# Kernel tuning notes

Hardware: AMD Instinct MI355X
Metric: run time of the kernel (lower is better)

Reference implementation:

```python
import jax, jax.numpy as jnp
import numpy as np

B, S, E, H = 2, 2048, 1024, 16
D = E // H  # head_dim = 64
FE = 4      # forward_expansion
EPS = 1e-5


def layernorm(x, g, b):
    mu = jnp.mean(x, axis=-1, keepdims=True)
    var = jnp.var(x, axis=-1, keepdims=True)
    return (x - mu) * jax.lax.rsqrt(var + EPS) * g + b


def setup_inputs() -> dict:
    key = jax.random.key(0)
    ks = jax.random.split(key, 16)
    s = lambda d: 1.0 / np.sqrt(d)
    return {
        "queries": jax.random.normal(ks[0], (B, S, E), jnp.float32),
        "keys": jax.random.normal(ks[1], (B, S, E), jnp.float32),
        "values": jax.random.normal(ks[2], (B, S, E), jnp.float32),
        "mask": jnp.ones((B, 1, S, S), jnp.int32),  # ignored (faithful to source bug)
        "Wq": jax.random.normal(ks[3], (D, D), jnp.float32) * s(D),
        "Wk": jax.random.normal(ks[4], (D, D), jnp.float32) * s(D),
        "Wv": jax.random.normal(ks[5], (D, D), jnp.float32) * s(D),
        "Wfc": jax.random.normal(ks[6], (E, E), jnp.float32) * s(E),
        "bfc": jnp.zeros((E,), jnp.float32),
        "W1": jax.random.normal(ks[7], (FE * E, E), jnp.float32) * s(E),
        "b1": jnp.zeros((FE * E,), jnp.float32),
        "W2": jax.random.normal(ks[8], (E, FE * E), jnp.float32) * s(FE * E),
        "b2": jnp.zeros((E,), jnp.float32),
        "ln1_g": jnp.ones((E,), jnp.float32),
        "ln1_b": jnp.zeros((E,), jnp.float32),
        "ln2_g": jnp.ones((E,), jnp.float32),
        "ln2_b": jnp.zeros((E,), jnp.float32),
    }


def reference(queries, keys, values, mask, Wq, Wk, Wv, Wfc, bfc, W1, b1, W2, b2,
              ln1_g, ln1_b, ln2_g, ln2_b):
    # --- MHA ---
    q = queries.reshape(B, S, H, D) @ Wq.T  # [B,S,H,D]
    k = keys.reshape(B, S, H, D) @ Wk.T
    v = values.reshape(B, S, H, D) @ Wv.T
    scores = jnp.einsum('bqhd,bkhd->bhqk', q, k)
    # source: softmax(scores / S**(-1/2)) == scores * sqrt(S)  (faithful quirk)
    # mask is ignored: source masked_fill is non-inplace and discarded
    attn = jax.nn.softmax(scores * jnp.sqrt(jnp.float32(S)), axis=-1)
    out = jnp.einsum('bhqk,bkhd->bqhd', attn, v).reshape(B, S, E)
    att = out @ Wfc.T + bfc
    # --- residual + LN + FFN + LN (dropout p=0 -> identity) ---
    h = layernorm(att + queries, ln1_g, ln1_b)
    x = jax.nn.relu(h @ W1.T + b1) @ W2.T + b2
    return layernorm(x + h, ln2_g, ln2_b)
```

## Files before the change

### kernel.cpp

```cpp
#include <hip/hip_runtime.h>
#include <hip/hip_bf16.h>
#include <math.h>

#define B_ 2
#define S_ 2048
#define E_ 1024
#define H_ 16
#define D_ 64
#define TOK (B_*S_)
#define SCALE2 (45.254833995939045f * 1.44269504088896340f)

typedef __bf16 bf16x8 __attribute__((ext_vector_type(8)));
typedef float floatx4 __attribute__((ext_vector_type(4)));
struct b4s { __hip_bfloat16 x, y, z, w; };

typedef const __attribute__((address_space(1))) char ga_char;
typedef __attribute__((address_space(3))) char ls_char;

__device__ __forceinline__ void gload_lds16(const void* g, ls_char* l) {
  __builtin_amdgcn_global_load_lds((ga_char*)g, l, 16, 0, 0);
}

#if __has_builtin(__builtin_amdgcn_exp2f)
#define EXP2(x) __builtin_amdgcn_exp2f(x)
#else
#define EXP2(x) exp2f(x)
#endif

#define SWZ(arr, half, row, qpos) \
  (*(bf16x8*)&arr[half][row][(((qpos) ^ ((row) & 3)) * 8)])

__device__ __forceinline__ void sbar() {
  asm volatile("" ::: "memory");
  __builtin_amdgcn_s_barrier();
  asm volatile("" ::: "memory");
}
#define VMW(n) asm volatile("s_waitcnt vmcnt(" #n ")" ::: "memory")

__global__ __launch_bounds__(256) void cast_all(
    const float* __restrict__ Wfc, const float* __restrict__ W1,
    const float* __restrict__ W2, __hip_bfloat16* __restrict__ Wfcb,
    __hip_bfloat16* __restrict__ W1b, __hip_bfloat16* __restrict__ W2b,
    const float* __restrict__ Wq, const float* __restrict__ Wk,
    const float* __restrict__ Wv, __hip_bfloat16* __restrict__ Whl) {
  const int i = blockIdx.x * 256 + threadIdx.x;
  if (i < 2359296) {
    const float* src; __hip_bfloat16* dst; int j;
    if (i < 262144)       { src = Wfc; dst = Wfcb; j = i; }
    else if (i < 1310720) { src = W1;  dst = W1b;  j = i - 262144; }
    else                  { src = W2;  dst = W2b;  j = i - 1310720; }
    float4 v = ((const float4*)src)[j];
    b4s o;
    o.x = __float2bfloat16(v.x); o.y = __float2bfloat16(v.y);
    o.z = __float2bfloat16(v.z); o.w = __float2bfloat16(v.w);
    *(b4s*)(dst + (size_t)j * 4) = o;
  } else if (i < 2362368) {
    const int idx = i - 2359296;
    const int m = idx >> 10;
    const int off = (idx & 1023) * 4;
    const float* W = (m == 0) ? Wq : (m == 1) ? Wk : Wv;
    float4 v = *(const float4*)(W + off);
    b4s hi, lo;
    hi.x = __float2bfloat16(v.x); lo.x = __float2bfloat16(v.x - __bfloat162float(hi.x));
    hi.y = __float2bfloat16(v.y); lo.y = __float2bfloat16(v.y - __bfloat162float(hi.y));
    hi.z = __float2bfloat16(v.z); lo.z = __float2bfloat16(v.z - __bfloat162float(hi.z));
    hi.w = __float2bfloat16(v.w); lo.w = __float2bfloat16(v.w - __bfloat162float(hi.w));
    *(b4s*)(Whl + (size_t)m * 8192 + off) = hi;
    *(b4s*)(Whl + (size_t)m * 8192 + 4096 + off) = lo;
  }
}

__global__ __launch_bounds__(256) void qkv_fused(
    const float* __restrict__ xq, const float* __restrict__ xk,
    const float* __restrict__ xv, const __hip_bfloat16* __restrict__ Whl,
    __hip_bfloat16* __restrict__ qhi, __hip_bfloat16* __restrict__ qlo,
    __hip_bfloat16* __restrict__ khi, __hip_bfloat16* __restrict__ klo,
    __hip_bfloat16* __restrict__ vt) {
  __shared__ __bf16 Xh[2][64][32], Xl[2][64][32];
  __shared__ __bf16 Vt[64][72];
  const int t = threadIdx.x, lane = t & 63, w = t >> 6;
  const int quad = lane >> 4, low = lane & 15;
  const int bh = blockIdx.y;
  const int b = bh >> 4, h = bh & 15;
  const int s0 = blockIdx.x * 64;
  const int sr = t >> 2;
  const int sc = (t & 3) * 16;
  const int scc = sc >> 5;
  const int p0 = (sc & 31) >> 3;

  for (int m = 0; m < 3; m++) {
    const float* xin = (m == 0) ? xq : (m == 1) ? xk : xv;
    const __hip_bfloat16* Wh = Whl + (size_t)m * 8192;
    const float sc_m = (m == 0) ? SCALE2 : 1.0f;

    __syncthreads();
    {
      const float* src = xin + ((size_t)(b * S_ + s0 + sr)) * E_ + h * 64 + sc;
      float4 f0 = *(const float4*)(src);
      float4 f1 = *(const float4*)(src + 4);
      float4 f2 = *(const float4*)(src + 8);
      float4 f3 = *(const float4*)(src + 12);
      float fv[16] = {f0.x, f0.y, f0.z, f0.w, f1.x, f1.y, f1.z, f1.w,
                      f2.x, f2.y, f2.z, f2.w, f3.x, f3.y, f3.z, f3.w};
      bf16x8 hi0, hi1, lo0, lo1;
      #pragma unroll
      for (int j = 0; j < 8; j++) {
        hi0[j] = (__bf16)fv[j];
        lo0[j] = (__bf16)(fv[j] - (float)hi0[j]);
        hi1[j] = (__bf16)fv[8 + j];
        lo1[j] = (__bf16)(fv[8 + j] - (float)hi1[j]);
      }
      SWZ(Xh, scc, sr, p0) = hi0;
      SWZ(Xh, scc, sr, p0 + 1) = hi1;
      SWZ(Xl, scc, sr, p0) = lo0;
      SWZ(Xl, scc, sr, p0 + 1) = lo1;
    }
    __syncthreads();

    bf16x8 ah[2], al[2];
    #pragma unroll
    for (int c = 0; c < 2; c++) {
      ah[c] = SWZ(Xh, c, w * 16 + low, quad);
      al[c] = SWZ(Xl, c, w * 16 + low, quad);
    }

    floatx4 acc[4];
    #pragma unroll
    for (int nn = 0; nn < 4; nn++) {
      floatx4 a = {};
      #pragma unroll
      for (int c = 0; c < 2; c++) {
        const __hip_bfloat16* wp = Wh + (nn * 16 + low) * 64 + c * 32 + quad * 8;
        bf16x8 wh_ = *(const bf16x8*)wp;
        bf16x8 wl_ = *(const bf16x8*)(wp + 4096);
        a = __builtin_amdgcn_mfma_f32_16x16x32_bf16(ah[c], wh_, a, 0, 0, 0);
        a = __builtin_amdgcn_mfma_f32_16x16x32_bf16(al[c], wh_, a, 0, 0, 0);
        a = __builtin_amdgcn_mfma_f32_16x16x32_bf16(ah[c], wl_, a, 0, 0, 0);
      }
      acc[nn] = a;
    }

    if (m < 2) {
      __hip_bfloat16* dh = (m == 0) ? qhi : khi;
      __hip_bfloat16* dl = (m == 0) ? qlo : klo;
      #pragma unroll
      for (int nn = 0; nn < 4; nn++) {
        #pragma unroll
        for (int i = 0; i < 4; i++) {
          const int s = s0 + w * 16 + quad * 4 + i;
          const int d = nn * 16 + low;
          const size_t adr = ((size_t)bh * S_ + s) * 64 + d;
          const float f = acc[nn][i] * sc_m;
          const __hip_bfloat16 hb = __float2bfloat16(f);
          dh[adr] = hb;
          dl[adr] = __float2bfloat16(f - __bfloat162float(hb));
        }
      }
    } else {
      #pragma unroll
      for (int nn = 0; nn < 4; nn++)
        #pragma unroll
        for (int i = 0; i < 4; i++)
          Vt[nn * 16 + low][w * 16 + quad * 4 + i] = (__bf16)acc[nn][i];
      __syncthreads();
      const int dr = t >> 2;
      const int scl = (t & 3) * 16;
      __hip_bfloat16* dst = vt + ((size_t)bh * 64 + dr) * S_ + s0 + scl;
      bf16x8 o0 = *(const bf16x8*)&Vt[dr][scl];
      bf16x8 o1 = *(const bf16x8*)&Vt[dr][scl + 8];
      *(bf16x8*)dst = o0;
      *(bf16x8*)(dst + 8) = o1;
    }
  }
}

__device__ __forceinline__ void softmax_update(
    const floatx4* sa, floatx4* oacc, float& mrow, float& lrow, bf16x8* pb) {
  float rmax;
  {
    float m0 = fmaxf(fmaxf(sa[0][0], sa[0][1]), fmaxf(sa[0][2], sa[0][3]));
    float m1 = fmaxf(fmaxf(sa[1][0], sa[1][1]), fmaxf(sa[1][2], sa[1][3]));
    float m2 = fmaxf(fmaxf(sa[2][0], sa[2][1]), fmaxf(sa[2][2], sa[2][3]));
    float m3 = fmaxf(fmaxf(sa[3][0], sa[3][1]), fmaxf(sa[3][2], sa[3][3]));
    rmax = fmaxf(fmaxf(m0, m1), fmaxf(m2, m3));
    rmax = fmaxf(rmax, __shfl_xor(rmax, 16, 64));
    rmax = fmaxf(rmax, __shfl_xor(rmax, 32, 64));
  }
  if (__any(rmax > mrow)) {
    const float nm = fmaxf(mrow, rmax);
    const float al = EXP2(mrow - nm);
    mrow = nm;
    lrow *= al;
    #pragma unroll
    for (int dt = 0; dt < 4; dt++) {
      oacc[dt][0] *= al; oacc[dt][1] *= al;
      oacc[dt][2] *= al; oacc[dt][3] *= al;
    }
  }
  float p[4][4];
  float rs;
  {
    float r0_ = 0.f, r1_ = 0.f, r2_ = 0.f, r3_ = 0.f;
    #pragma unroll
    for (int i = 0; i < 4; i++) {
      p[0][i] = EXP2(sa[0][i] - mrow); r0_ += p[0][i];
      p[1][i] = EXP2(sa[1][i] - mrow); r1_ += p[1][i];
      p[2][i] = EXP2(sa[2][i] - mrow); r2_ += p[2][i];
      p[3][i] = EXP2(sa[3][i] - mrow); r3_ += p[3][i];
    }
    rs = (r0_ + r1_) + (r2_ + r3_);
    rs += __shfl_xor(rs, 16, 64);
    rs += __shfl_xor(rs, 32, 64);
  }
  lrow += rs;
  #pragma unroll
  for (int kh2 = 0; kh2 < 2; kh2++) {
    bf16x8 v;
    v[0] = (__bf16)p[kh2][0]; v[1] = (__bf16)p[kh2][1];
    v[2] = (__bf16)p[kh2][2]; v[3] = (__bf16)p[kh2][3];
    v[4] = (__bf16)p[kh2 + 2][0]; v[5] = (__bf16)p[kh2 + 2][1];
    v[6] = (__bf16)p[kh2 + 2][2]; v[7] = (__bf16)p[kh2 + 2][3];
    pb[kh2] = v;
  }
}

__global__ __launch_bounds__(512, 4) void attn_mfma(
    const __hip_bfloat16* __restrict__ Qhi, const __hip_bfloat16* __restrict__ Qlo,
    const __hip_bfloat16* __restrict__ Khi, const __hip_bfloat16* __restrict__ Klo,
    const __hip_bfloat16* __restrict__ Vtg, __hip_bfloat16* __restrict__ ctx) {
  __shared__ __bf16 Kh[2][2][64][32], Kl[2][2][64][32], Vs[2][2][64][32];
  const int t = threadIdx.x, lane = t & 63, w = t >> 6;
  const int quad = lane >> 4, low = lane & 15;
  const int bh = blockIdx.x;
  const int qw = blockIdx.y * 128 + w * 16;

  const int sh = w >> 2;
  const int r0 = (w & 3) * 16;
  const int srow = r0 + (lane >> 2);
  const int sq = (lane & 3) ^ (srow & 3);
  const __hip_bfloat16* gK = Khi + ((size_t)bh * S_ + srow) * 64 + sh * 32 + sq * 8;
  const __hip_bfloat16* gL = Klo + ((size_t)bh * S_ + srow) * 64 + sh * 32 + sq * 8;
  const __hip_bfloat16* gV = Vtg + ((size_t)bh * 64 + srow) * S_ + sh * 32 + sq * 8;

  bf16x8 qh[2], ql[2];
  {
    const size_t qbase = ((size_t)bh * S_ + qw + low) * 64 + quad * 8;
    qh[0] = *(const bf16x8*)(Qhi + qbase);
    qh[1] = *(const bf16x8*)(Qhi + qbase + 32);
    ql[0] = *(const bf16x8*)(Qlo + qbase);
    ql[1] = *(const bf16x8*)(Qlo + qbase + 32);
  }

  floatx4 oacc[4] = {};
  float mrow = -3e38f, lrow = 0.f;

  gload_lds16(gK, (ls_char*)&Kh[0][sh][r0][0]);
  gload_lds16(gL, (ls_char*)&Kl[0][sh][r0][0]);
  gload_lds16(gV, (ls_char*)&Vs[0][sh][r0][0]);

  for (int kt = 0; kt < S_ / 64; kt++) {
    const int cur = kt & 1;
    __syncthreads();
    if (kt + 1 < S_ / 64) {
      gload_lds16(gK + (size_t)(kt + 1) * 4096, (ls_char*)&Kh[cur ^ 1][sh][r0][0]);
      gload_lds16(gL + (size_t)(kt + 1) * 4096, (ls_char*)&Kl[cur ^ 1][sh][r0][0]);
      gload_lds16(gV + (size_t)(kt + 1) * 64,   (ls_char*)&Vs[cur ^ 1][sh][r0][0]);
    }

    floatx4 sa[4];
    __builtin_amdgcn_s_setprio(1);
    #pragma unroll
    for (int nn = 0; nn < 4; nn++) {
      const int prow = (nn & 1) * 32 + (nn >> 1) * 4 + (low >> 2) * 8 + (low & 3);
      bf16x8 kh0 = SWZ(Kh[cur], 0, prow, quad);
      bf16x8 kh1 = SWZ(Kh[cur], 1, prow, quad);
      bf16x8 kl0 = SWZ(Kl[cur], 0, prow, quad);
      bf16x8 kl1 = SWZ(Kl[cur], 1, prow, quad);
      floatx4 s = {};
      s = __builtin_amdgcn_mfma_f32_16x16x32_bf16(kh0, qh[0], s, 0, 0, 0);
      s = __builtin_amdgcn_mfma_f32_16x16x32_bf16(kh1, qh[1], s, 0, 0, 0);
      s = __builtin_amdgcn_mfma_f32_16x16x32_bf16(kl0, qh[0], s, 0, 0, 0);
      s = __builtin_amdgcn_mfma_f32_16x16x32_bf16(kl1, qh[1], s, 0, 0, 0);
      s = __builtin_amdgcn_mfma_f32_16x16x32_bf16(kh0, ql[0], s, 0, 0, 0);
      s = __builtin_amdgcn_mfma_f32_16x16x32_bf16(kh1, ql[1], s, 0, 0, 0);
      sa[nn] = s;
    }
    __builtin_amdgcn_s_setprio(0);

    bf16x8 pb[2];
    softmax_update(sa, oacc, mrow, lrow, pb);

    __builtin_amdgcn_s_setprio(1);
    #pragma unroll
    for (int dt = 0; dt < 4; dt++) {
      bf16x8 vb0 = SWZ(Vs[cur], 0, dt * 16 + low, quad);
      bf16x8 vb1 = SWZ(Vs[cur], 1, dt * 16 + low, quad);
      oacc[dt] = __builtin_amdgcn_mfma_f32_16x16x32_bf16(vb0, pb[0], oacc[dt], 0, 0, 0);
      oacc[dt] = __builtin_amdgcn_mfma_f32_16x16x32_bf16(vb1, pb[1], oacc[dt], 0, 0, 0);
    }
    __builtin_amdgcn_s_setprio(0);
  }

  const float inv = 1.0f / lrow;
  const int b = bh >> 4, h = bh & 15;
  const size_t base = ((size_t)(b * S_ + qw + low)) * E_ + h * 64 + quad * 4;
  #pragma unroll
  for (int dt = 0; dt < 4; dt++) {
    b4s o;
    o.x = __float2bfloat16(oacc[dt][0] * inv);
    o.y = __float2bfloat16(oacc[dt][1] * inv);
    o.z = __float2bfloat16(oacc[dt][2] * inv);
    o.w = __float2bfloat16(oacc[dt][3] * inv);
    *(b4s*)(ctx + base + dt * 16) = o;
  }
}

template <int RELU, int OUT_BF16, int PARTIAL>
__global__ __launch_bounds__(256) void gemm_mfma(
    const __hip_bfloat16* __restrict__ A, const __hip_bfloat16* __restrict__ Wt,
    const float* __restrict__ bias, void* __restrict__ C0, void* __restrict__ C1,
    int M, int N, int Kblk, int lda) {
  __shared__ __bf16 As[2][128][64];
  __shared__ __bf16 Bs[2][128][64];
  const int t = threadIdx.x;
  const int lane = t & 63;
  const int w = t >> 6;
  const int wr = w >> 1, wc = w & 1;
  const int m0 = blockIdx.y * 128, n0 = blockIdx.x * 128;
  void* Cout = (blockIdx.z == 0) ? C0 : C1;

  A += (size_t)blockIdx.z * Kblk;
  Wt += (size_t)blockIdx.z * Kblk;

  floatx4 acc[4][4] = {};
  const int srow = t >> 3;
  const int ssc = ((t & 7) ^ (srow & 7)) * 8;

  const __hip_bfloat16* gA = A + (size_t)(m0 + srow) * lda + ssc;
  const __hip_bfloat16* gB = Wt + (size_t)(n0 + srow) * lda + ssc;
  const size_t rstep = (size_t)32 * lda;

#define GSTAGE(buf, k0) do {                                      \
    ls_char* lA = (ls_char*)&As[buf][0][0] + w * 1024;            \
    ls_char* lB = (ls_char*)&Bs[buf][0][0] + w * 1024;            \
    gload_lds16(gA + (k0),             lA);                       \
    gload_lds16(gA + (k0) + rstep,     lA + 4096);                \
    gload_lds16(gA + (k0) + 2 * rstep, lA + 8192);                \
    gload_lds16(gA + (k0) + 3 * rstep, lA + 12288);               \
    gload_lds16(gB + (k0),             lB);                       \
    gload_lds16(gB + (k0) + rstep,     lB + 4096);                \
    gload_lds16(gB + (k0) + 2 * rstep, lB + 8192);                \
    gload_lds16(gB + (k0) + 3 * rstep, lB + 12288);               \
  } while (0)

  GSTAGE(0, 0);
  const int nsteps = Kblk >> 6;
  for (int st = 0; st < nsteps; st++) {
    const int cur = st & 1;
    __syncthreads();
    if (st + 1 < nsteps) GSTAGE(cur ^ 1, (st + 1) * 64);

    #pragma unroll
    for (int ks = 0; ks < 2; ks++) {
      bf16x8 af[4], bfr[4];
      #pragma unroll
      for (int i = 0; i < 4; i++) {
        const int ra = wr * 64 + i * 16 + (lane & 15);
        const int ca = (((lane >> 4) + ks * 4) ^ (ra & 7)) * 8;
        af[i] = *(const bf16x8*)&As[cur][ra][ca];
        const int rb = wc * 64 + i * 16 + (lane & 15);
        const int cb = (((lane >> 4) + ks * 4) ^ (rb & 7)) * 8;
        bfr[i] = *(const bf16x8*)&Bs[cur][rb][cb];
      }
      #pragma unroll
      for (int mi = 0; mi < 4; mi++)
        #pragma unroll
        for (int ni = 0; ni < 4; ni++)
          acc[mi][ni] = __builtin_amdgcn_mfma_f32_16x16x32_bf16(
              af[mi], bfr[ni], acc[mi][ni], 0, 0, 0);
    }
  }
#undef GSTAGE

  const int cil = lane & 15;
  const int quad = lane >> 4;
  #pragma unroll
  for (int ni = 0; ni < 4; ni++) {
    const int col = n0 + wc * 64 + ni * 16 + cil;
    const float bb = PARTIAL ? 0.f : bias[col];
    #pragma unroll
    for (int mi = 0; mi < 4; mi++) {
      const int row = m0 + wr * 64 + mi * 16 + quad * 4;
      #pragma unroll
      for (int i = 0; i < 4; i++) {
        if (PARTIAL) {
          ((float*)Cout)[(size_t)(row + i) * N + col] = acc[mi][ni][i];
        } else {
          float vv = acc[mi][ni][i] + bb;
          if (RELU) vv = fmaxf(vv, 0.f);
          if (OUT_BF16)
            ((__hip_bfloat16*)Cout)[(size_t)(row + i) * N + col] = __float2bfloat16(vv);
          else
            ((float*)Cout)[(size_t)(row + i) * N + col] = vv;
        }
      }
    }
  }
}

__global__ __launch_bounds__(512, 2) void gemm_ff1(
    const __hip_bfloat16* __restrict__ A, const __hip_bfloat16* __restrict__ Wt,
    const float* __restrict__ bias, __hip_bfloat16* __restrict__ C) {
  __shared__ __bf16 As[2][256][64];
  __shared__ __bf16 Bs[2][256][64];
  const int t = threadIdx.x, lane = t & 63, w = t >> 6;
  const int quad = lane >> 4, low = lane & 15;
  const int wm = w >> 2, wn = w & 3;
  const int m0 = blockIdx.y * 256, n0 = blockIdx.x * 256;

  floatx4 acc[8][4] = {};

  const int srow = t >> 3;
  const int ssc = ((t & 7) ^ (srow & 7)) * 8;
  const __hip_bfloat16* gA = A + (size_t)(m0 + srow) * 1024 + ssc;
  const __hip_bfloat16* gB = Wt + (size_t)(n0 + srow) * 1024 + ssc;

#define LA(buf) ((ls_char*)&As[buf][0][0] + w * 1024)
#define LB(buf) ((ls_char*)&Bs[buf][0][0] + w * 1024)
#define ST_A0(buf, k0) do {                                   \
    gload_lds16(gA + (k0),          LA(buf));                 \
    gload_lds16(gA + (k0) + 131072, LA(buf) + 16384);         \
  } while (0)
#define ST_A1(buf, k0) do {                                   \
    gload_lds16(gA + (k0) + 65536,  LA(buf) + 8192);          \
    gload_lds16(gA + (k0) + 196608, LA(buf) + 24576);         \
  } while (0)
#define ST_B0(buf, k0) do {                                   \
    gload_lds16(gB + (k0),          LB(buf));                 \
    gload_lds16(gB + (k0) + 65536,  LB(buf) + 8192);          \
  } while (0)
#define ST_B1(buf, k0) do {                                   \
    gload_lds16(gB + (k0) + 131072, LB(buf) + 16384);         \
    gload_lds16(gB + (k0) + 196608, LB(buf) + 24576);         \
  } while (0)

#define LDA_HALF(mh) do {                                                     \
    _Pragma("unroll")                                                         \
    for (int mi = 0; mi < 4; mi++) {                                          \
      const int ra = wm * 128 + (mh) * 64 + mi * 16 + low;                    \
      af[mi][0] = *(const bf16x8*)&As[cur][ra][((quad) ^ (ra & 7)) * 8];      \
      af[mi][1] = *(const bf16x8*)&As[cur][ra][((4 + quad) ^ (ra & 7)) * 8];  \
    }                                                                         \
  } while (0)

#define LDB_HALF(dst, nh) do {                                                \
    _Pragma("unroll")                                                         \
    for (int ni = 0; ni < 2; ni++) {                                          \
      const int rb = (nh) * 128 + wn * 32 + ni * 16 + low;                    \
      dst[ni][0] = *(const bf16x8*)&Bs[cur][rb][((quad) ^ (rb & 7)) * 8];     \
      dst[ni][1] = *(const bf16x8*)&Bs[cur][rb][((4 + quad) ^ (rb & 7)) * 8]; \
    }                                                                         \
  } while (0)

#define MFMA_Q(bfr, mh, nh) do {                                              \
    __builtin_amdgcn_s_setprio(1);                                            \
    _Pragma("unroll")                                                         \
    for (int mi = 0; mi < 4; mi++)                                            \
      _Pragma("unroll")                                                       \
      for (int ni = 0; ni < 2; ni++) {                                        \
        acc[(mh)*4+mi][(nh)*2+ni] = __builtin_amdgcn_mfma_f32_16x16x32_bf16(  \
            af[mi][0], bfr[ni][0], acc[(mh)*4+mi][(nh)*2+ni], 0, 0, 0);       \
        acc[(mh)*4+mi][(nh)*2+ni] = __builtin_amdgcn_mfma_f32_16x16x32_bf16(  \
            af[mi][1], bfr[ni][1], acc[(mh)*4+mi][(nh)*2+ni], 0, 0, 0);       \
      }                                                                       \
    __builtin_amdgcn_s_setprio(0);                                            \
  } while (0)

  ST_A0(0, 0); ST_B0(0, 0); ST_B1(0, 0); ST_A1(0, 0);

  bf16x8 af[4][2], bA[2][2], bB[2][2];

  for (int kt = 0; kt < 16; kt++) {
    const int cur = kt & 1, nxt = cur ^ 1;
    const int kn = (kt + 1) * 64;
    const bool more = (kt + 1 < 16);

    VMW(4);
    sbar();
    LDA_HALF(0);
    LDB_HALF(bA, 0);
    if (more) ST_A0(nxt, kn);
    MFMA_Q(bA, 0, 0);

    if (kt < 15) { VMW(4); } else { VMW(2); }
    sbar();
    LDB_HALF(bB, 1);
    if (more) ST_B0(nxt, kn);
    MFMA_Q(bB, 0, 1);

    if (kt < 15) { VMW(4); } else { VMW(0); }
    sbar();
    LDA_HALF(1);
    if (more) ST_B1(nxt, kn);
    MFMA_Q(bB, 1, 1);

    sbar();
    if (more) ST_A1(nxt, kn);
    MFMA_Q(bA, 1, 0);
  }
#undef ST_A0
#undef ST_A1
#undef ST_B0
#undef ST_B1
#undef LA
#undef LB
#undef LDA_HALF
#undef LDB_HALF
#undef MFMA_Q

  #pragma unroll
  for (int n4 = 0; n4 < 4; n4++) {
    const int nh = n4 >> 1, ni = n4 & 1;
    const int col = n0 + nh * 128 + wn * 32 + ni * 16 + low;
    const float bb = bias[col];
    #pragma unroll
    for (int mi = 0; mi < 8; mi++) {
      const int row = m0 + wm * 128 + mi * 16 + quad * 4;
      #pragma unroll
      for (int i = 0; i < 4; i++) {
        float vv = fmaxf(acc[mi][n4][i] + bb, 0.f);
        C[(size_t)(row + i) * 4096 + col] = __float2bfloat16(vv);
      }
    }
  }
}

template <int EMIT_BF16, int HAS_A1, int HAS_BIAS>
__global__ __launch_bounds__(256) void add_ln(
    const float* __restrict__ a0, const float* __restrict__ a1,
    const float* __restrict__ r, const float* __restrict__ bias,
    const float* __restrict__ g, const float* __restrict__ bt,
    float* __restrict__ out, __hip_bfloat16* __restrict__ outb) {
  __shared__ float red[16];
  const int tok = blockIdx.x, t = threadIdx.x;
  float4 av = ((const float4*)(a0 + (size_t)tok * E_))[t];
  float4 rv = ((const float4*)(r + (size_t)tok * E_))[t];
  float4 x;
  x.x = av.x + rv.x; x.y = av.y + rv.y; x.z = av.z + rv.z; x.w = av.w + rv.w;
  if (HAS_A1) {
    float4 a2 = ((const float4*)(a1 + (size_t)tok * E_))[t];
    x.x += a2.x; x.y += a2.y; x.z += a2.z; x.w += a2.w;
  }
  if (HAS_BIAS) {
    float4 cv = ((const float4*)bias)[t];
    x.x += cv.x; x.y += cv.y; x.z += cv.z; x.w += cv.w;
  }
  float sum = x.x + x.y + x.z + x.w;
  float ssq = x.x * x.x + x.y * x.y + x.z * x.z + x.w * x.w;
  #pragma unroll
  for (int off = 32; off >= 1; off >>= 1) {
    sum += __shfl_down(sum, off, 64);
    ssq += __shfl_down(ssq, off, 64);
  }
  const int wave = t >> 6;
  if ((t & 63) == 0) { red[wave] = sum; red[4 + wave] = ssq; }
  __syncthreads();
  if (t == 0) {
    float s = red[0] + red[1] + red[2] + red[3];
    float qq = red[4] + red[5] + red[6] + red[7];
    float mu = s * (1.0f / E_);
    red[8] = mu;
    red[9] = qq * (1.0f / E_) - mu * mu;
  }
  __syncthreads();
  const float mu = red[8];
  const float inv = rsqrtf(red[9] + 1e-5f);
  float4 gv = ((const float4*)g)[t];
  float4 bv = ((const float4*)bt)[t];
  float4 o;
  o.x = (x.x - mu) * inv * gv.x + bv.x;
  o.y = (x.y - mu) * inv * gv.y + bv.y;
  o.z = (x.z - mu) * inv * gv.z + bv.z;
  o.w = (x.w - mu) * inv * gv.w + bv.w;
  ((float4*)(out + (size_t)tok * E_))[t] = o;
  if (EMIT_BF16) {
    b4s ob;
    ob.x = __float2bfloat16(o.x); ob.y = __float2bfloat16(o.y);
    ob.z = __float2bfloat16(o.z); ob.w = __float2bfloat16(o.w);
    *(b4s*)(outb + (size_t)tok * E_ + t * 4) = ob;
  }
}

extern "C" void kernel_launch(void* const* d_in, const int* in_sizes, int n_in,
                              void* d_out, int out_size, void* d_ws, size_t ws_size,
                              hipStream_t stream) {
  const float* queries = (const float*)d_in[0];
  const float* keys    = (const float*)d_in[1];
  const float* values  = (const float*)d_in[2];
  const float* Wq  = (const float*)d_in[4];
  const float* Wk  = (const float*)d_in[5];
  const float* Wv  = (const float*)d_in[6];
  const float* Wfc = (const float*)d_in[7];
  const float* bfc = (const float*)d_in[8];
  const float* W1  = (const float*)d_in[9];
  const float* b1  = (const float*)d_in[10];
  const float* W2  = (const float*)d_in[11];
  const float* b2  = (const float*)d_in[12];
  const float* ln1_g = (const float*)d_in[13];
  const float* ln1_b = (const float*)d_in[14];
  const float* ln2_g = (const float*)d_in[15];
  const float* ln2_b = (const float*)d_in[16];

  const size_t M1 = 1048576;
  float* ws = (float*)d_ws;
  float* P0  = ws;
  float* P1  = ws + 4 * M1;
  float* Hf  = ws + 8 * M1;
  __hip_bfloat16* bb = (__hip_bfloat16*)(ws + 12 * M1);
  __hip_bfloat16* CTXb = bb;
  __hip_bfloat16* Hb   = bb + 4 * M1;
  __hip_bfloat16* Wfcb = bb + 8 * M1;
  __hip_bfloat16* W1b  = bb + 9 * M1;
  __hip_bfloat16* W2b  = bb + 13 * M1;
  __hip_bfloat16* Qhi  = bb + 17 * M1;
  __hip_bfloat16* Qlo  = bb + 21 * M1;
  __hip_bfloat16* Khi  = bb + 25 * M1;
  __hip_bfloat16* Klo  = bb + 29 * M1;
  __hip_bfloat16* Vtb  = bb + 33 * M1;
  __hip_bfloat16* FF1b = bb + 17 * M1;
  __hip_bfloat16* Whlb = bb + 37 * M1;
  float* out = (float*)d_out;

  cast_all<<<9228, 256, 0, stream>>>(Wfc, W1, W2, Wfcb, W1b, W2b,
                                     Wq, Wk, Wv, Whlb);

  qkv_fused<<<dim3(S_ / 64, B_ * H_), 256, 0, stream>>>(
      queries, keys, values, Whlb, Qhi, Qlo, Khi, Klo, Vtb);
  attn_mfma<<<dim3(B_ * H_, S_ / 128), 512, 0, stream>>>(
      Qhi, Qlo, Khi, Klo, Vtb, CTXb);
  gemm_mfma<0, 0, 1><<<dim3(E_ / 128, TOK / 128, 2), 256, 0, stream>>>(
      CTXb, Wfcb, nullptr, P0, P1, TOK, E_, 512, E_);
  add_ln<1, 1, 1><<<TOK, 256, 0, stream>>>(
      P0, P1, queries, bfc, ln1_g, ln1_b, Hf, Hb);
  gemm_ff1<<<dim3(4 * E_ / 256, TOK / 256), 512, 0, stream>>>(
      Hb, W1b, b1, FF1b);
  gemm_mfma<0, 0, 1><<<dim3(E_ / 128, TOK / 128, 2), 256, 0, stream>>>(
      FF1b, W2b, nullptr, P0, P1, TOK, E_, 2048, 4 * E_);
  add_ln<0, 1, 1><<<TOK, 256, 0, stream>>>(
      P0, P1, Hf, b2, ln2_g, ln2_b, out, nullptr);
}
```

Before: 377.2 us.

## Split GEMM K-tile into half-stages with finer-grained async LDS pipelining

Restructures the GEMM main loop so each 64-wide K tile is split into two 32-wide halves stored in separate LDS sub-buffers. Each half waits only on its own global-to-LDS loads via a partial vmcnt wait, issues the next tile's matching half-load, and then runs its MFMAs under raised wave priority. The aim is to overlap global loads with MFMA work more tightly and shorten load-to-use stalls. In exchange there are twice as many barriers per K step and a different swizzle layout, which could add synchronization overhead.

```diff
diff --git a/kernel.cpp b/kernel.cpp
--- a/kernel.cpp
+++ b/kernel.cpp
@@ -320,11 +320,12 @@
     const __hip_bfloat16* __restrict__ A, const __hip_bfloat16* __restrict__ Wt,
     const float* __restrict__ bias, void* __restrict__ C0, void* __restrict__ C1,
     int M, int N, int Kblk, int lda) {
-  __shared__ __bf16 As[2][128][64];
-  __shared__ __bf16 Bs[2][128][64];
+  __shared__ __bf16 As[2][2][128][32];
+  __shared__ __bf16 Bs[2][2][128][32];
   const int t = threadIdx.x;
   const int lane = t & 63;
   const int w = t >> 6;
+  const int quad = lane >> 4, low = lane & 15;
   const int wr = w >> 1, wc = w & 1;
   const int m0 = blockIdx.y * 128, n0 = blockIdx.x * 128;
   void* Cout = (blockIdx.z == 0) ? C0 : C1;
@@ -333,57 +334,75 @@
   Wt += (size_t)blockIdx.z * Kblk;
 
   floatx4 acc[4][4] = {};
-  const int srow = t >> 3;
-  const int ssc = ((t & 7) ^ (srow & 7)) * 8;
+  const int srow = t >> 2;
+  const int ssc = ((t & 3) ^ (srow & 3)) * 8;
 
   const __hip_bfloat16* gA = A + (size_t)(m0 + srow) * lda + ssc;
   const __hip_bfloat16* gB = Wt + (size_t)(n0 + srow) * lda + ssc;
-  const size_t rstep = (size_t)32 * lda;
-
-#define GSTAGE(buf, k0) do {                                      \
-    ls_char* lA = (ls_char*)&As[buf][0][0] + w * 1024;            \
-    ls_char* lB = (ls_char*)&Bs[buf][0][0] + w * 1024;            \
-    gload_lds16(gA + (k0),             lA);                       \
-    gload_lds16(gA + (k0) + rstep,     lA + 4096);                \
-    gload_lds16(gA + (k0) + 2 * rstep, lA + 8192);                \
-    gload_lds16(gA + (k0) + 3 * rstep, lA + 12288);               \
-    gload_lds16(gB + (k0),             lB);                       \
-    gload_lds16(gB + (k0) + rstep,     lB + 4096);                \
-    gload_lds16(gB + (k0) + 2 * rstep, lB + 8192);                \
-    gload_lds16(gB + (k0) + 3 * rstep, lB + 12288);               \
-  } while (0)
-
-  GSTAGE(0, 0);
+  const size_t rstep = (size_t)64 * lda;
+
+#define STA(buf, kh, k0) do {                                     \
+    ls_char* l = (ls_char*)&As[buf][kh][0][0] + w * 1024;         \
+    gload_lds16(gA + (k0),         l);                            \
+    gload_lds16(gA + (k0) + rstep, l + 4096);                     \
+  } while (0)
+#define STB(buf, kh, k0) do {                                     \
+    ls_char* l = (ls_char*)&Bs[buf][kh][0][0] + w * 1024;         \
+    gload_lds16(gB + (k0),         l);                            \
+    gload_lds16(gB + (k0) + rstep, l + 4096);                     \
+  } while (0)
+
+  STA(0, 0, 0); STB(0, 0, 0); STA(0, 1, 32); STB(0, 1, 32);
+
   const int nsteps = Kblk >> 6;
   for (int st = 0; st < nsteps; st++) {
-    const int cur = st & 1;
-    __syncthreads();
-    if (st + 1 < nsteps) GSTAGE(cur ^ 1, (st + 1) * 64);
-
-    #pragma unroll
-    for (int ks = 0; ks < 2; ks++) {
-      bf16x8 af[4], bfr[4];
-      #pragma unroll
-      for (int i = 0; i < 4; i++) {
-        const int ra = wr * 64 + i * 16 + (lane & 15);
-        const int ca = (((lane >> 4) + ks * 4) ^ (ra & 7)) * 8;
-        af[i] = *(const bf16x8*)&As[cur][ra][ca];
-        const int rb = wc * 64 + i * 16 + (lane & 15);
-        const int cb = (((lane >> 4) + ks * 4) ^ (rb & 7)) * 8;
-        bfr[i] = *(const bf16x8*)&Bs[cur][rb][cb];
-      }
-      #pragma unroll
-      for (int mi = 0; mi < 4; mi++)
-        #pragma unroll
-        for (int ni = 0; ni < 4; ni++)
-          acc[mi][ni] = __builtin_amdgcn_mfma_f32_16x16x32_bf16(
-              af[mi], bfr[ni], acc[mi][ni], 0, 0, 0);
-    }
-  }
-#undef GSTAGE
+    const int cur = st & 1, nxt = cur ^ 1;
+    const bool more = (st + 1 < nsteps);
+    const int kn = (st + 1) * 64;
+
+    VMW(4);
+    sbar();
+    bf16x8 af[4], bfr[4];
+    #pragma unroll
+    for (int i = 0; i < 4; i++) {
+      const int ra = wr * 64 + i * 16 + low;
+      af[i] = *(const bf16x8*)&As[cur][0][ra][(quad ^ (ra & 3)) * 8];
+      const int rb = wc * 64 + i * 16 + low;
+      bfr[i] = *(const bf16x8*)&Bs[cur][0][rb][(quad ^ (rb & 3)) * 8];
+    }
+    if (more) { STA(nxt, 0, kn); STB(nxt, 0, kn); }
+    __builtin_amdgcn_s_setprio(1);
+    #pragma unroll
+    for (int mi = 0; mi < 4; mi++)
+      #pragma unroll
+      for (int ni = 0; ni < 4; ni++)
+        acc[mi][ni] = __builtin_amdgcn_mfma_f32_16x16x32_bf16(
+            af[mi], bfr[ni], acc[mi][ni], 0, 0, 0);
+    __builtin_amdgcn_s_setprio(0);
+
+    if (more) { VMW(4); } else { VMW(0); }
+    sbar();
+    #pragma unroll
+    for (int i = 0; i < 4; i++) {
+      const int ra = wr * 64 + i * 16 + low;
+      af[i] = *(const bf16x8*)&As[cur][1][ra][(quad ^ (ra & 3)) * 8];
+      const int rb = wc * 64 + i * 16 + low;
+      bfr[i] = *(const bf16x8*)&Bs[cur][1][rb][(quad ^ (rb & 3)) * 8];
+    }
+    if (more) { STA(nxt, 1, kn + 32); STB(nxt, 1, kn + 32); }
+    __builtin_amdgcn_s_setprio(1);
+    #pragma unroll
+    for (int mi = 0; mi < 4; mi++)
+      #pragma unroll
+      for (int ni = 0; ni < 4; ni++)
+        acc[mi][ni] = __builtin_amdgcn_mfma_f32_16x16x32_bf16(
+            af[mi], bfr[ni], acc[mi][ni], 0, 0, 0);
+    __builtin_amdgcn_s_setprio(0);
+  }
+#undef STA
+#undef STB
 
   const int cil = lane & 15;
-  const int quad = lane >> 4;
   #pragma unroll
   for (int ni = 0; ni < 4; ni++) {
     const int col = n0 + wc * 64 + ni * 16 + cil;
```

Result: no change. 381.2 us (+1.1%).

## Add dedicated pipelined 256x128 split-K GEMM kernel for FFN second layer

Applied to the files above, without the earlier changes.

Replaces the generic gemm_mfma call for the FF2 projection with a specialized 512-thread kernel that uses 256x128 output tiles, split-K over two halves, double-buffered LDS filled via global_load_lds, and interleaved quarter-step loads/MFMAs with waitcnt barriers. The intent is to overlap global-to-LDS prefetch with MFMA work and raise per-block reuse compared to the 128x128 generic kernel. The larger tile halves the number of blocks (128 total), which may reduce occupancy and wave-level parallelism across CUs.

```diff
diff --git a/kernel.cpp b/kernel.cpp
--- a/kernel.cpp
+++ b/kernel.cpp
@@ -535,6 +535,126 @@
   }
 }
 
+__global__ __launch_bounds__(512, 1) void gemm_ff2(
+    const __hip_bfloat16* __restrict__ A, const __hip_bfloat16* __restrict__ Wt,
+    float* __restrict__ C0, float* __restrict__ C1) {
+  __shared__ __bf16 As[2][256][64];
+  __shared__ __bf16 Bs[2][128][64];
+  const int t = threadIdx.x, lane = t & 63, w = t >> 6;
+  const int quad = lane >> 4, low = lane & 15;
+  const int wm = w >> 2, wn = w & 3;
+  const int m0 = blockIdx.y * 256, n0 = blockIdx.x * 128;
+  float* Cout = blockIdx.z ? C1 : C0;
+  const int LDA = 4096;
+
+  floatx4 acc[8][2] = {};
+
+  const int srow = t >> 3;
+  const int ssc = ((t & 7) ^ (srow & 7)) * 8;
+  const __hip_bfloat16* gA = A + (size_t)(m0 + srow) * LDA
+                               + (size_t)blockIdx.z * 2048 + ssc;
+  const __hip_bfloat16* gB = Wt + (size_t)(n0 + srow) * LDA
+                               + (size_t)blockIdx.z * 2048 + ssc;
+
+#define LA2(buf) ((ls_char*)&As[buf][0][0] + w * 1024)
+#define LB2(buf) ((ls_char*)&Bs[buf][0][0] + w * 1024)
+#define F2_A0(buf, k0) do {                                         \
+    gload_lds16(gA + (k0),                    LA2(buf));            \
+    gload_lds16(gA + (k0) + (size_t)128*LDA,  LA2(buf) + 16384);    \
+  } while (0)
+#define F2_A1(buf, k0) do {                                         \
+    gload_lds16(gA + (k0) + (size_t)64*LDA,   LA2(buf) + 8192);     \
+    gload_lds16(gA + (k0) + (size_t)192*LDA,  LA2(buf) + 24576);    \
+  } while (0)
+#define F2_B0(buf, k0) do {                                         \
+    gload_lds16(gB + (k0),                    LB2(buf));            \
+  } while (0)
+#define F2_B1(buf, k0) do {                                         \
+    gload_lds16(gB + (k0) + (size_t)64*LDA,   LB2(buf) + 8192);     \
+  } while (0)
+
+#define LDA2_HALF(mh) do {                                                    \
+    _Pragma("unroll")                                                         \
+    for (int mi = 0; mi < 4; mi++) {                                          \
+      const int ra = wm * 128 + (mh) * 64 + mi * 16 + low;                    \
+      af[mi][0] = *(const bf16x8*)&As[cur][ra][((quad) ^ (ra & 7)) * 8];      \
+      af[mi][1] = *(const bf16x8*)&As[cur][ra][((4 + quad) ^ (ra & 7)) * 8];  \
+    }                                                                         \
+  } while (0)
+
+#define LDB2_HALF(dst, nh) do {                                               \
+    const int rb = (nh) * 64 + wn * 16 + low;                                 \
+    dst[0] = *(const bf16x8*)&Bs[cur][rb][((quad) ^ (rb & 7)) * 8];           \
+    dst[1] = *(const bf16x8*)&Bs[cur][rb][((4 + quad) ^ (rb & 7)) * 8];       \
+  } while (0)
+
+#define MFMA_Q2(bfr, mh, nh) do {                                             \
+    __builtin_amdgcn_s_setprio(1);                                            \
+    _Pragma("unroll")                                                         \
+    for (int mi = 0; mi < 4; mi++) {                                          \
+      acc[(mh)*4+mi][nh] = __builtin_amdgcn_mfma_f32_16x16x32_bf16(           \
+          af[mi][0], bfr[0], acc[(mh)*4+mi][nh], 0, 0, 0);                    \
+      acc[(mh)*4+mi][nh] = __builtin_amdgcn_mfma_f32_16x16x32_bf16(           \
+          af[mi][1], bfr[1], acc[(mh)*4+mi][nh], 0, 0, 0);                    \
+    }                                                                         \
+    __builtin_amdgcn_s_setprio(0);                                            \
+  } while (0)
+
+  F2_A0(0, 0); F2_B0(0, 0); F2_B1(0, 0); F2_A1(0, 0);
+
+  bf16x8 af[4][2], bA[2], bB[2];
+
+  for (int kt = 0; kt < 32; kt++) {
+    const int cur = kt & 1, nxt = cur ^ 1;
+    const int kn = (kt + 1) * 64;
+    const bool more = (kt + 1 < 32);
+
+    VMW(3);
+    sbar();
+    LDA2_HALF(0);
+    LDB2_HALF(bA, 0);
+    if (more) F2_A0(nxt, kn);
+    MFMA_Q2(bA, 0, 0);
+
+    if (more) { VMW(4); } else { VMW(2); }
+    sbar();
+    LDB2_HALF(bB, 1);
+    if (more) F2_B0(nxt, kn);
+    MFMA_Q2(bB, 0, 1);
+
+    if (more) { VMW(3); } else { VMW(0); }
+    sbar();
+    LDA2_HALF(1);
+    if (more) F2_B1(nxt, kn);
+    MFMA_Q2(bB, 1, 1);
+
+    sbar();
+    if (more) F2_A1(nxt, kn);
+    MFMA_Q2(bA, 1, 0);
+  }
+#undef F2_A0
+#undef F2_A1
+#undef F2_B0
+#undef F2_B1
+#undef LA2
+#undef LB2
+#undef LDA2_HALF
+#undef LDB2_HALF
+#undef MFMA_Q2
+
+  #pragma unroll
+  for (int nh = 0; nh < 2; nh++) {
+    const int col = n0 + nh * 64 + wn * 16 + low;
+    #pragma unroll
+    for (int mi = 0; mi < 8; mi++) {
+      const int row = m0 + wm * 128 + mi * 16 + quad * 4;
+      #pragma unroll
+      for (int i = 0; i < 4; i++)
+        Cout[(size_t)(row + i) * E_ + col] = acc[mi][nh][i];
+    }
+  }
+}
+
 template <int EMIT_BF16, int HAS_A1, int HAS_BIAS>
 __global__ __launch_bounds__(256) void add_ln(
     const float* __restrict__ a0, const float* __restrict__ a1,
@@ -644,8 +764,8 @@
       P0, P1, queries, bfc, ln1_g, ln1_b, Hf, Hb);
   gemm_ff1<<<dim3(4 * E_ / 256, TOK / 256), 512, 0, stream>>>(
       Hb, W1b, b1, FF1b);
-  gemm_mfma<0, 0, 1><<<dim3(E_ / 128, TOK / 128, 2), 256, 0, stream>>>(
-      FF1b, W2b, nullptr, P0, P1, TOK, E_, 2048, 4 * E_);
+  gemm_ff2<<<dim3(E_ / 128, TOK / 256, 2), 512, 0, stream>>>(
+      FF1b, W2b, P0, P1);
   add_ln<0, 1, 1><<<TOK, 256, 0, stream>>>(
       P0, P1, Hf, b2, ln2_g, ln2_b, out, nullptr);
 }
```

Measured after the change: 381.6 us. Within noise of the previous version (+1.2%).

## Use 256x256-tile split-K GEMM for FF2 with four partial buffers

Applied to the files above, without the earlier changes.

Generalizes the FF1 256x256 tile kernel into a template that handles both FF1 (fused bias+ReLU, bf16 output) and FF2, which now runs as a split-K of 4 with fp32 partials. The final add+LayerNorm sums four partials instead of two. The workspace is remapped so the extra partial buffers reuse dead Q/K and CTX regions. Occupancy hint drops from 2 to 1 block per CU, and the extra partials raise fp32 write and read traffic in exchange for larger-tile reuse in FF2.

```diff
diff --git a/kernel.cpp b/kernel.cpp
--- a/kernel.cpp
+++ b/kernel.cpp
@@ -408,40 +408,44 @@
   }
 }
 
-__global__ __launch_bounds__(512, 2) void gemm_ff1(
+template <int LDAK, int NSTR, int FUSED>
+__global__ __launch_bounds__(512, 1) void gemm_256(
     const __hip_bfloat16* __restrict__ A, const __hip_bfloat16* __restrict__ Wt,
-    const float* __restrict__ bias, __hip_bfloat16* __restrict__ C) {
+    const float* __restrict__ bias, __hip_bfloat16* __restrict__ Cb,
+    float* __restrict__ P0_, float* __restrict__ P1_,
+    float* __restrict__ P2_, float* __restrict__ P3_) {
   __shared__ __bf16 As[2][256][64];
   __shared__ __bf16 Bs[2][256][64];
   const int t = threadIdx.x, lane = t & 63, w = t >> 6;
   const int quad = lane >> 4, low = lane & 15;
   const int wm = w >> 2, wn = w & 3;
   const int m0 = blockIdx.y * 256, n0 = blockIdx.x * 256;
+  const int z = blockIdx.z;
 
   floatx4 acc[8][4] = {};
 
   const int srow = t >> 3;
   const int ssc = ((t & 7) ^ (srow & 7)) * 8;
-  const __hip_bfloat16* gA = A + (size_t)(m0 + srow) * 1024 + ssc;
-  const __hip_bfloat16* gB = Wt + (size_t)(n0 + srow) * 1024 + ssc;
+  const __hip_bfloat16* gA = A + (size_t)(m0 + srow) * LDAK + (size_t)z * 1024 + ssc;
+  const __hip_bfloat16* gB = Wt + (size_t)(n0 + srow) * LDAK + (size_t)z * 1024 + ssc;
 
 #define LA(buf) ((ls_char*)&As[buf][0][0] + w * 1024)
 #define LB(buf) ((ls_char*)&Bs[buf][0][0] + w * 1024)
-#define ST_A0(buf, k0) do {                                   \
-    gload_lds16(gA + (k0),          LA(buf));                 \
-    gload_lds16(gA + (k0) + 131072, LA(buf) + 16384);         \
-  } while (0)
-#define ST_A1(buf, k0) do {                                   \
-    gload_lds16(gA + (k0) + 65536,  LA(buf) + 8192);          \
-    gload_lds16(gA + (k0) + 196608, LA(buf) + 24576);         \
-  } while (0)
-#define ST_B0(buf, k0) do {                                   \
-    gload_lds16(gB + (k0),          LB(buf));                 \
-    gload_lds16(gB + (k0) + 65536,  LB(buf) + 8192);          \
-  } while (0)
-#define ST_B1(buf, k0) do {                                   \
-    gload_lds16(gB + (k0) + 131072, LB(buf) + 16384);         \
-    gload_lds16(gB + (k0) + 196608, LB(buf) + 24576);         \
+#define ST_A0(buf, k0) do {                                            \
+    gload_lds16(gA + (k0),                      LA(buf));              \
+    gload_lds16(gA + (k0) + (size_t)128 * LDAK, LA(buf) + 16384);      \
+  } while (0)
+#define ST_A1(buf, k0) do {                                            \
+    gload_lds16(gA + (k0) + (size_t)64 * LDAK,  LA(buf) + 8192);       \
+    gload_lds16(gA + (k0) + (size_t)192 * LDAK, LA(buf) + 24576);      \
+  } while (0)
+#define ST_B0(buf, k0) do {                                            \
+    gload_lds16(gB + (k0),                      LB(buf));              \
+    gload_lds16(gB + (k0) + (size_t)64 * LDAK,  LB(buf) + 8192);       \
+  } while (0)
+#define ST_B1(buf, k0) do {                                            \
+    gload_lds16(gB + (k0) + (size_t)128 * LDAK, LB(buf) + 16384);      \
+    gload_lds16(gB + (k0) + (size_t)192 * LDAK, LB(buf) + 24576);      \
   } while (0)
 
 #define LDA_HALF(mh) do {                                                     \
@@ -518,26 +522,32 @@
 #undef LDB_HALF
 #undef MFMA_Q
 
+  float* Pz = (z == 0) ? P0_ : (z == 1) ? P1_ : (z == 2) ? P2_ : P3_;
   #pragma unroll
   for (int n4 = 0; n4 < 4; n4++) {
     const int nh = n4 >> 1, ni = n4 & 1;
     const int col = n0 + nh * 128 + wn * 32 + ni * 16 + low;
-    const float bb = bias[col];
+    const float bb = FUSED ? bias[col] : 0.f;
     #pragma unroll
     for (int mi = 0; mi < 8; mi++) {
       const int row = m0 + wm * 128 + mi * 16 + quad * 4;
       #pragma unroll
       for (int i = 0; i < 4; i++) {
-        float vv = fmaxf(acc[mi][n4][i] + bb, 0.f);
-        C[(size_t)(row + i) * 4096 + col] = __float2bfloat16(vv);
+        if (FUSED) {
+          float vv = fmaxf(acc[mi][n4][i] + bb, 0.f);
+          Cb[(size_t)(row + i) * NSTR + col] = __float2bfloat16(vv);
+        } else {
+          Pz[(size_t)(row + i) * NSTR + col] = acc[mi][n4][i];
+        }
       }
     }
   }
 }
 
-template <int EMIT_BF16, int HAS_A1, int HAS_BIAS>
+template <int EMIT_BF16, int NA, int HAS_BIAS>
 __global__ __launch_bounds__(256) void add_ln(
     const float* __restrict__ a0, const float* __restrict__ a1,
+    const float* __restrict__ a2, const float* __restrict__ a3,
     const float* __restrict__ r, const float* __restrict__ bias,
     const float* __restrict__ g, const float* __restrict__ bt,
     float* __restrict__ out, __hip_bfloat16* __restrict__ outb) {
@@ -547,9 +557,15 @@
   float4 rv = ((const float4*)(r + (size_t)tok * E_))[t];
   float4 x;
   x.x = av.x + rv.x; x.y = av.y + rv.y; x.z = av.z + rv.z; x.w = av.w + rv.w;
-  if (HAS_A1) {
-    float4 a2 = ((const float4*)(a1 + (size_t)tok * E_))[t];
-    x.x += a2.x; x.y += a2.y; x.z += a2.z; x.w += a2.w;
+  if (NA >= 2) {
+    float4 v = ((const float4*)(a1 + (size_t)tok * E_))[t];
+    x.x += v.x; x.y += v.y; x.z += v.z; x.w += v.w;
+  }
+  if (NA >= 4) {
+    float4 v2 = ((const float4*)(a2 + (size_t)tok * E_))[t];
+    float4 v3 = ((const float4*)(a3 + (size_t)tok * E_))[t];
+    x.x += v2.x + v3.x; x.y += v2.y + v3.y;
+    x.z += v2.z + v3.z; x.w += v2.w + v3.w;
   }
   if (HAS_BIAS) {
     float4 cv = ((const float4*)bias)[t];
@@ -621,14 +637,16 @@
   __hip_bfloat16* Hb   = bb + 4 * M1;
   __hip_bfloat16* Wfcb = bb + 8 * M1;
   __hip_bfloat16* W1b  = bb + 9 * M1;
-  __hip_bfloat16* W2b  = bb + 13 * M1;
-  __hip_bfloat16* Qhi  = bb + 17 * M1;
-  __hip_bfloat16* Qlo  = bb + 21 * M1;
-  __hip_bfloat16* Khi  = bb + 25 * M1;
-  __hip_bfloat16* Klo  = bb + 29 * M1;
-  __hip_bfloat16* Vtb  = bb + 33 * M1;
+  __hip_bfloat16* Qhi  = bb + 13 * M1;
+  __hip_bfloat16* Qlo  = bb + 17 * M1;
+  __hip_bfloat16* Khi  = bb + 21 * M1;
+  __hip_bfloat16* Klo  = bb + 25 * M1;
+  __hip_bfloat16* Vtb  = bb + 29 * M1;
   __hip_bfloat16* FF1b = bb + 17 * M1;
+  __hip_bfloat16* W2b  = bb + 33 * M1;
   __hip_bfloat16* Whlb = bb + 37 * M1;
+  float* P2 = (float*)bb;
+  float* P3 = (float*)(bb + 9 * M1);
   float* out = (float*)d_out;
 
   cast_all<<<9228, 256, 0, stream>>>(Wfc, W1, W2, Wfcb, W1b, W2b,
@@ -640,12 +658,12 @@
       Qhi, Qlo, Khi, Klo, Vtb, CTXb);
   gemm_mfma<0, 0, 1><<<dim3(E_ / 128, TOK / 128, 2), 256, 0, stream>>>(
       CTXb, Wfcb, nullptr, P0, P1, TOK, E_, 512, E_);
-  add_ln<1, 1, 1><<<TOK, 256, 0, stream>>>(
-      P0, P1, queries, bfc, ln1_g, ln1_b, Hf, Hb);
-  gemm_ff1<<<dim3(4 * E_ / 256, TOK / 256), 512, 0, stream>>>(
-      Hb, W1b, b1, FF1b);
-  gemm_mfma<0, 0, 1><<<dim3(E_ / 128, TOK / 128, 2), 256, 0, stream>>>(
-      FF1b, W2b, nullptr, P0, P1, TOK, E_, 2048, 4 * E_);
-  add_ln<0, 1, 1><<<TOK, 256, 0, stream>>>(
-      P0, P1, Hf, b2, ln2_g, ln2_b, out, nullptr);
-}
+  add_ln<1, 2, 1><<<TOK, 256, 0, stream>>>(
+      P0, P1, nullptr, nullptr, queries, bfc, ln1_g, ln1_b, Hf, Hb);
+  gemm_256<1024, 4096, 1><<<dim3(4 * E_ / 256, TOK / 256, 1), 512, 0, stream>>>(
+      Hb, W1b, b1, FF1b, nullptr, nullptr, nullptr, nullptr);
+  gemm_256<4096, 1024, 0><<<dim3(E_ / 256, TOK / 256, 4), 512, 0, stream>>>(
+      FF1b, W2b, nullptr, nullptr, P0, P1, P2, P3);
+  add_ln<0, 4, 1><<<TOK, 256, 0, stream>>>(
+      P0, P1, P2, P3, Hf, b2, ln2_g, ln2_b, out, nullptr);
+}
```

New measurement: 377.7 us. Within noise of the previous version (+0.1%).
